# Optimization experiments

Hardware: AMD Instinct MI355X
Metric: run time of the kernel (lower is better)

The kernel has to match this reference:

```python
import jax, jax.numpy as jnp
import numpy as np

N = 100000   # nodes
E = 3200000  # edges (avg degree 32)
IN = 128     # in_channels
H = 128      # hidden_channels
G = 512      # graphs in batch


def setup_inputs() -> dict:
    key = jax.random.key(0)
    ks = jax.random.split(key, 8)
    x = jax.random.normal(ks[0], (N, IN), dtype=jnp.float32)
    edge_index = jax.random.randint(ks[1], (2, E), 0, N, dtype=jnp.int64)
    batch = jnp.sort(jax.random.randint(ks[2], (N,), 0, G, dtype=jnp.int64))
    s_in = 1.0 / np.sqrt(IN)
    s_h = 1.0 / np.sqrt(H)
    W1 = jax.random.normal(ks[3], (IN, H), dtype=jnp.float32) * s_in
    b1 = jnp.zeros((H,), dtype=jnp.float32)
    W2 = jax.random.normal(ks[4], (H, H), dtype=jnp.float32) * s_h
    b2 = jnp.zeros((H,), dtype=jnp.float32)
    Wc = jax.random.normal(ks[5], (H, 1), dtype=jnp.float32) * s_h
    bc = jnp.zeros((1,), dtype=jnp.float32)
    return {"x": x, "edge_index": edge_index, "batch": batch,
            "W1": W1, "b1": b1, "W2": W2, "b2": b2, "Wc": Wc, "bc": bc}


def _gcn_conv(x, W, b, src, dst, n):
    # PyG GCNConv: x' = D^{-1/2} (A+I) D^{-1/2} X W + b  (self-loops already in src/dst)
    h = x @ W                                      # [n, H] small GEMM
    ones = jnp.ones(src.shape[0], dtype=h.dtype)
    deg = jax.ops.segment_sum(ones, dst, num_segments=n)
    dinv = jnp.where(deg > 0, jax.lax.rsqrt(deg), 0.0)
    norm = dinv[src] * dinv[dst]                   # [E+n]
    msgs = h[src] * norm[:, None]                  # gather + scale (memory-bound)
    return jax.ops.segment_sum(msgs, dst, num_segments=n) + b


def reference(x, edge_index, batch, W1, b1, W2, b2, Wc, bc):
    n = x.shape[0]
    loop = jnp.arange(n, dtype=edge_index.dtype)
    src = jnp.concatenate([edge_index[0], loop])   # add self-loops
    dst = jnp.concatenate([edge_index[1], loop])
    h = jax.nn.relu(_gcn_conv(x, W1, b1, src, dst, n))
    h = jax.nn.relu(_gcn_conv(h, W2, b2, src, dst, n))
    # global_mean_pool: segment mean over graph ids
    counts = jax.ops.segment_sum(jnp.ones(n, dtype=h.dtype), batch, num_segments=G)
    sums = jax.ops.segment_sum(h, batch, num_segments=G)
    pooled = sums / jnp.maximum(counts, 1.0)[:, None]   # [G, H]
    return jax.nn.sigmoid(pooled @ Wc + bc)             # [G, 1]
```

## Files before the change

### kernel.cpp

```cpp
#include <hip/hip_runtime.h>

typedef unsigned short ushort_t;
typedef unsigned int uint_t;
typedef unsigned char u8_t;

typedef __bf16 bf16x8 __attribute__((ext_vector_type(8)));
typedef float f32x4 __attribute__((ext_vector_type(4)));
typedef uint_t uint32x4 __attribute__((ext_vector_type(4)));
typedef uint_t uint32x2 __attribute__((ext_vector_type(2)));
typedef _Float16 h2 __attribute__((ext_vector_type(2)));

#define EPB 5120
#define NSH 9
#define MSK 511
#define BPAD 4104

__device__ __forceinline__ float b2f(ushort_t u) {
    union { uint_t ui; float f; } c; c.ui = ((uint_t)u) << 16; return c.f;
}
__device__ __forceinline__ ushort_t f2b(float f) {
    union { float f; uint_t ui; } c; c.f = f;
    uint_t u = c.ui;
    uint_t r = (u + 0x7fffu + ((u >> 16) & 1u)) >> 16;
    return (ushort_t)r;
}
__device__ __forceinline__ u8_t f2e5(float x) {
    ushort_t h = __builtin_bit_cast(ushort_t, (_Float16)x);
    uint_t r = ((uint_t)h + 0x7Fu + ((h >> 8) & 1u)) >> 8;
    return (u8_t)r;
}
__device__ __forceinline__ void upk_add(uint_t d, h2* acc) {
    uint_t A = __builtin_amdgcn_perm(0u, d, 0x010C000Cu);
    uint_t B = __builtin_amdgcn_perm(0u, d, 0x030C020Cu);
    acc[0] += __builtin_bit_cast(h2, A);
    acc[1] += __builtin_bit_cast(h2, B);
}

__global__ __launch_bounds__(256) void p1_hist(const int* __restrict__ dst,
                                               int* __restrict__ H,
                                               const float* __restrict__ W1,
                                               const float* __restrict__ W2,
                                               ushort_t* __restrict__ W1t,
                                               ushort_t* __restrict__ W2t,
                                               u8_t* __restrict__ h8z,
                                               int E, int NBLK, int B, int N) {
    int t = threadIdx.x, c = blockIdx.x;
    if (c >= NBLK + 128) {
        if (t < 32) ((uint_t*)h8z)[(size_t)N * 32 + t] = 0u;
        return;
    }
    if (c >= NBLK) {
        int idx = (c - NBLK) * 256 + t;
        int sel = idx >> 14;
        int i = idx & 16383;
        int k = i >> 7, nn = i & 127;
        const float* S = sel ? W2 : W1;
        ushort_t* D = sel ? W2t : W1t;
        D[nn * 128 + k] = f2b(S[k * 128 + nn]);
        return;
    }
    __shared__ int hist[256];
    if (t < 256) hist[t] = 0;
    __syncthreads();
    int base = c * EPB;
    int lim = min(E - base, EPB);
    for (int i = t; i < lim; i += 256)
        atomicAdd(&hist[dst[base + i] >> NSH], 1);
    __syncthreads();
    if (t < B) H[t * NBLK + c] = hist[t];
}

__global__ __launch_bounds__(256) void reduce256(const int* __restrict__ in,
                                                 int* __restrict__ bsums, int n) {
    __shared__ int s[256];
    int t = threadIdx.x, g = blockIdx.x * 256 + t;
    s[t] = (g < n) ? in[g] : 0;
    __syncthreads();
    for (int o = 128; o > 0; o >>= 1) {
        if (t < o) s[t] += s[t + o];
        __syncthreads();
    }
    if (t == 0) bsums[blockIdx.x] = s[0];
}

__global__ __launch_bounds__(512) void scan_small(const int* __restrict__ in,
                                                  int* __restrict__ outEx, int n) {
    __shared__ int s[512];
    int t = threadIdx.x;
    int v = (t < n) ? in[t] : 0;
    s[t] = v;
    __syncthreads();
    for (int o = 1; o < 512; o <<= 1) {
        int x = 0;
        if (t >= o) x = s[t - o];
        __syncthreads();
        s[t] += x;
        __syncthreads();
    }
    if (t < n) outEx[t] = s[t] - v;
}

__global__ __launch_bounds__(256) void scan256ex(const int* __restrict__ in,
                                                 const int* __restrict__ boffs,
                                                 int* __restrict__ outEx, int n) {
    __shared__ int s[256];
    int t = threadIdx.x, g = blockIdx.x * 256 + t;
    int v = (g < n) ? in[g] : 0;
    s[t] = v;
    __syncthreads();
    for (int o = 1; o < 256; o <<= 1) {
        int x = 0;
        if (t >= o) x = s[t - o];
        __syncthreads();
        s[t] += x;
        __syncthreads();
    }
    if (g < n) outEx[g] = boffs[blockIdx.x] + s[t] - v;
}

__global__ __launch_bounds__(256) void p3_scatter(const int* __restrict__ src,
                                                  const int* __restrict__ dst,
                                                  const int* __restrict__ Hex,
                                                  uint_t* __restrict__ packed,
                                                  int E, int NBLK, int B) {
    __shared__ int offsL[256];
    __shared__ int cur[256];
    int t = threadIdx.x, c = blockIdx.x;
    if (t < B) {
        offsL[t] = Hex[t * NBLK + c];
        cur[t] = 0;
    }
    __syncthreads();
    int base = c * EPB;
    int lim = min(E - base, EPB);
    for (int i = t; i < lim; i += 256) {
        int d = dst[base + i];
        int s = src[base + i];
        int b = d >> NSH;
        int r = atomicAdd(&cur[b], 1);
        packed[offsL[b] + r] = ((uint_t)s << NSH) | (uint_t)(d & MSK);
    }
}

__global__ __launch_bounds__(512) void p4_build(const uint_t* __restrict__ packed,
                                                const int* __restrict__ Hex,
                                                int* __restrict__ adj,
                                                int* __restrict__ offs,
                                                int* __restrict__ dgr,
                                                float* __restrict__ dinv,
                                                int E, int N, int NBLK, int B) {
    __shared__ int dcnt[512], loc[512], cur[512], sps[512];
    int t = threadIdx.x, b = blockIdx.x;
    int bs = Hex[b * NBLK];
    int be = (b + 1 < B) ? Hex[(b + 1) * NBLK] : E;
    int m = be - bs;
    dcnt[t] = 0;
    __syncthreads();
    for (int i = t; i < m; i += 512)
        atomicAdd(&dcnt[packed[bs + i] & MSK], 1);
    __syncthreads();
    int d = dcnt[t];
    int pd = (d + 8) & ~7;
    sps[t] = pd;
    __syncthreads();
    for (int o = 1; o < 512; o <<= 1) {
        int x = 0;
        if (t >= o) x = sps[t - o];
        __syncthreads();
        sps[t] += x;
        __syncthreads();
    }
    int bsp = ((bs + 7) & ~7) + b * BPAD;
    int ex = sps[t] - pd;
    int node = b * 512 + t;
    if (node < N) {
        int nbase = bsp + ex;
        offs[node] = nbase;
        dgr[node]  = pd;
        dinv[node] = rsqrtf((float)(d + 1));
        adj[nbase] = node;
        for (int i = d + 1; i < pd; ++i)
            adj[nbase + i] = N;
    }
    loc[t] = ex + 1;
    cur[t] = 0;
    __syncthreads();
    for (int i = t; i < m; i += 512) {
        uint_t p = packed[bs + i];
        int l = p & MSK;
        int r = atomicAdd(&cur[l], 1);
        adj[bsp + loc[l] + r] = (int)(p >> NSH);
    }
}

__global__ __launch_bounds__(256, 4) void gemm_scale(const ushort_t* __restrict__ Xin,
                                                     const ushort_t* __restrict__ Wt,
                                                     const float* __restrict__ dinv,
                                                     u8_t* __restrict__ Hout8, int n) {
    __shared__ ushort_t lds[128 * 136];
    int tid = threadIdx.x;
    for (int i = tid; i < 128 * 16; i += 256) {
        int r = i >> 4, c8 = (i & 15) << 3;
        *(uint32x4*)(lds + r * 136 + c8) = *(const uint32x4*)(Wt + r * 128 + c8);
    }
    __syncthreads();
    int lane = tid & 63, wave = tid >> 6;
    int m = lane & 15, q = lane >> 4;
    int row0 = blockIdx.x * 64 + wave * 16;
    int ar = row0 + m;
    if (ar > n - 1) ar = n - 1;
    bf16x8 a[4];
#pragma unroll
    for (int ks = 0; ks < 4; ++ks)
        a[ks] = __builtin_bit_cast(bf16x8,
            *(const uint32x4*)(Xin + (size_t)ar * 128 + ks * 32 + q * 8));
    f32x4 acc[8];
    f32x4 zero = {0.f, 0.f, 0.f, 0.f};
#pragma unroll
    for (int nt = 0; nt < 8; ++nt) acc[nt] = zero;
#pragma unroll
    for (int nt = 0; nt < 8; ++nt) {
#pragma unroll
        for (int ks = 0; ks < 4; ++ks) {
            bf16x8 b = __builtin_bit_cast(bf16x8,
                *(const uint32x4*)(lds + (nt * 16 + m) * 136 + ks * 32 + q * 8));
            acc[nt] = __builtin_amdgcn_mfma_f32_16x16x32_bf16(a[ks], b, acc[nt], 0, 0, 0);
        }
    }
    float dv[4];
#pragma unroll
    for (int r = 0; r < 4; ++r) {
        int gr = row0 + q * 4 + r;
        dv[r] = (gr < n) ? dinv[gr] : 0.f;
    }
#pragma unroll
    for (int nt = 0; nt < 8; ++nt) {
#pragma unroll
        for (int r = 0; r < 4; ++r) {
            int gr = row0 + q * 4 + r;
            if (gr < n)
                Hout8[(size_t)gr * 128 + nt * 16 + m] = f2e5(acc[nt][r] * dv[r]);
        }
    }
}

__global__ __launch_bounds__(256, 4) void gemm_scale_f32(const float* __restrict__ Xf,
                                                         const ushort_t* __restrict__ Wt,
                                                         const float* __restrict__ dinv,
                                                         u8_t* __restrict__ Hout8, int n) {
    __shared__ ushort_t lds[128 * 136];
    int tid = threadIdx.x;
    for (int i = tid; i < 128 * 16; i += 256) {
        int r = i >> 4, c8 = (i & 15) << 3;
        *(uint32x4*)(lds + r * 136 + c8) = *(const uint32x4*)(Wt + r * 128 + c8);
    }
    __syncthreads();
    int lane = tid & 63, wave = tid >> 6;
    int m = lane & 15, q = lane >> 4;
    int row0 = blockIdx.x * 64 + wave * 16;
    int ar = row0 + m;
    if (ar > n - 1) ar = n - 1;
    bf16x8 a[4];
#pragma unroll
    for (int ks = 0; ks < 4; ++ks) {
        const float* p = Xf + (size_t)ar * 128 + ks * 32 + q * 8;
        f32x4 lo = *(const f32x4*)p;
        f32x4 hi = *(const f32x4*)(p + 4);
        ushort_t t[8];
        t[0] = f2b(lo[0]); t[1] = f2b(lo[1]); t[2] = f2b(lo[2]); t[3] = f2b(lo[3]);
        t[4] = f2b(hi[0]); t[5] = f2b(hi[1]); t[6] = f2b(hi[2]); t[7] = f2b(hi[3]);
        a[ks] = __builtin_bit_cast(bf16x8, *(uint32x4*)t);
    }
    f32x4 acc[8];
    f32x4 zero = {0.f, 0.f, 0.f, 0.f};
#pragma unroll
    for (int nt = 0; nt < 8; ++nt) acc[nt] = zero;
#pragma unroll
    for (int nt = 0; nt < 8; ++nt) {
#pragma unroll
        for (int ks = 0; ks < 4; ++ks) {
            bf16x8 b = __builtin_bit_cast(bf16x8,
                *(const uint32x4*)(lds + (nt * 16 + m) * 136 + ks * 32 + q * 8));
            acc[nt] = __builtin_amdgcn_mfma_f32_16x16x32_bf16(a[ks], b, acc[nt], 0, 0, 0);
        }
    }
    float dv[4];
#pragma unroll
    for (int r = 0; r < 4; ++r) {
        int gr = row0 + q * 4 + r;
        dv[r] = (gr < n) ? dinv[gr] : 0.f;
    }
#pragma unroll
    for (int nt = 0; nt < 8; ++nt) {
#pragma unroll
        for (int r = 0; r < 4; ++r) {
            int gr = row0 + q * 4 + r;
            if (gr < n)
                Hout8[(size_t)gr * 128 + nt * 16 + m] = f2e5(acc[nt][r] * dv[r]);
        }
    }
}

__device__ __forceinline__ void agg_core(const u8_t* __restrict__ Hs8,
                                         const int* __restrict__ adj,
                                         int beg, int pd, int g, uint_t colb,
                                         h2* acc) {
    int e = 0;
    for (; e + 16 <= pd; e += 16) {
        const int4 sv = *(const int4*)(adj + beg + e + g * 4);
        uint_t o0 = ((uint_t)sv.x << 7) | colb;
        uint_t o1 = ((uint_t)sv.y << 7) | colb;
        uint_t o2 = ((uint_t)sv.z << 7) | colb;
        uint_t o3 = ((uint_t)sv.w << 7) | colb;
        uint32x2 w0 = *(const uint32x2*)(Hs8 + o0);
        uint32x2 w1 = *(const uint32x2*)(Hs8 + o1);
        uint32x2 w2 = *(const uint32x2*)(Hs8 + o2);
        uint32x2 w3 = *(const uint32x2*)(Hs8 + o3);
        upk_add(w0[0], acc); upk_add(w0[1], acc + 2);
        upk_add(w1[0], acc); upk_add(w1[1], acc + 2);
        upk_add(w2[0], acc); upk_add(w2[1], acc + 2);
        upk_add(w3[0], acc); upk_add(w3[1], acc + 2);
    }
    if (e < pd) {
        const int2 sv = *(const int2*)(adj + beg + e + g * 2);
        uint_t o0 = ((uint_t)sv.x << 7) | colb;
        uint_t o1 = ((uint_t)sv.y << 7) | colb;
        uint32x2 w0 = *(const uint32x2*)(Hs8 + o0);
        uint32x2 w1 = *(const uint32x2*)(Hs8 + o1);
        upk_add(w0[0], acc); upk_add(w0[1], acc + 2);
        upk_add(w1[0], acc); upk_add(w1[1], acc + 2);
    }
}

__device__ __forceinline__ void slot_reduce(h2* acc) {
#pragma unroll
    for (int k = 0; k < 4; ++k) {
        uint_t v = __builtin_bit_cast(uint_t, acc[k]);
        acc[k] += __builtin_bit_cast(h2, (uint_t)__shfl_xor(v, 16, 64));
        v = __builtin_bit_cast(uint_t, acc[k]);
        acc[k] += __builtin_bit_cast(h2, (uint_t)__shfl_xor(v, 32, 64));
    }
}

__global__ __launch_bounds__(256, 4) void agg_kernel(const u8_t* __restrict__ Hs8,
                                                     const int* __restrict__ adj,
                                                     const int* __restrict__ offs,
                                                     const int* __restrict__ dgr,
                                                     const float* __restrict__ dinv,
                                                     const float* __restrict__ bias,
                                                     ushort_t* __restrict__ Out, int n) {
    int node = blockIdx.x * 4 + (threadIdx.x >> 6);
    if (node >= n) return;
    int lane = threadIdx.x & 63;
    int g = lane >> 4;
    int l16 = lane & 15;
    uint_t colb = (uint_t)l16 * 8;
    const int beg = offs[node];
    const int pd  = dgr[node];
    h2 acc[4];
    h2 hz = {(_Float16)0.f, (_Float16)0.f};
#pragma unroll
    for (int k = 0; k < 4; ++k) acc[k] = hz;
    agg_core(Hs8, adj, beg, pd, g, colb, acc);
    slot_reduce(acc);
    if (g == 0) {
        float di = dinv[node];
        ushort_t o[8];
#pragma unroll
        for (int k = 0; k < 4; ++k) {
            float f0 = (float)acc[k][0];
            float f1 = (float)acc[k][1];
            o[2 * k]     = f2b(fmaxf(di * f0 + bias[colb + 2 * k], 0.f));
            o[2 * k + 1] = f2b(fmaxf(di * f1 + bias[colb + 2 * k + 1], 0.f));
        }
        *(uint32x4*)(Out + (size_t)node * 128 + colb) = *(uint32x4*)o;
    }
}

__global__ __launch_bounds__(256, 4) void agg_pool_kernel(const u8_t* __restrict__ Hs8,
                                                          const int* __restrict__ adj,
                                                          const int* __restrict__ offs,
                                                          const int* __restrict__ dgr,
                                                          const float* __restrict__ dinv,
                                                          const float* __restrict__ bias,
                                                          const float* __restrict__ Wc,
                                                          float* __restrict__ Sout, int n) {
    int node = blockIdx.x * 4 + (threadIdx.x >> 6);
    if (node >= n) return;
    int lane = threadIdx.x & 63;
    int g = lane >> 4;
    int l16 = lane & 15;
    uint_t colb = (uint_t)l16 * 8;
    const int beg = offs[node];
    const int pd  = dgr[node];
    h2 acc[4];
    h2 hz = {(_Float16)0.f, (_Float16)0.f};
#pragma unroll
    for (int k = 0; k < 4; ++k) acc[k] = hz;
    agg_core(Hs8, adj, beg, pd, g, colb, acc);
    slot_reduce(acc);
    float local = 0.f;
    float di = dinv[node];
#pragma unroll
    for (int k = 0; k < 4; ++k) {
        float f0 = fmaxf(di * (float)acc[k][0] + bias[colb + 2 * k], 0.f);
        float f1 = fmaxf(di * (float)acc[k][1] + bias[colb + 2 * k + 1], 0.f);
        local += f0 * Wc[colb + 2 * k] + f1 * Wc[colb + 2 * k + 1];
    }
    local += __shfl_xor(local, 1, 64);
    local += __shfl_xor(local, 2, 64);
    local += __shfl_xor(local, 4, 64);
    local += __shfl_xor(local, 8, 64);
    if (lane == 0) Sout[node] = local;
}

__global__ __launch_bounds__(256) void pool2_kernel(const float* __restrict__ S,
                                                    const int* __restrict__ batch,
                                                    const float* __restrict__ bc,
                                                    float* __restrict__ out, int n) {
    int g = blockIdx.x;
    int t = threadIdx.x;
    int lo = 0, hi = n;
    while (lo < hi) { int mid = (lo + hi) >> 1; if (batch[mid] < g) lo = mid + 1; else hi = mid; }
    int start = lo;
    hi = n;
    while (lo < hi) { int mid = (lo + hi) >> 1; if (batch[mid] < g + 1) lo = mid + 1; else hi = mid; }
    int stop = lo;
    float s = 0.f;
    for (int i = start + t; i < stop; i += 256) s += S[i];
    __shared__ float red[256];
    red[t] = s;
    __syncthreads();
    for (int o = 128; o > 0; o >>= 1) {
        if (t < o) red[t] += red[t + o];
        __syncthreads();
    }
    if (t == 0) {
        int cg = stop - start;
        float z = red[0] / (float)(cg > 0 ? cg : 1) + bc[0];
        out[g] = 1.f / (1.f + expf(-z));
    }
}

extern "C" void kernel_launch(void* const* d_in, const int* in_sizes, int n_in,
                              void* d_out, int out_size, void* d_ws, size_t ws_size,
                              hipStream_t stream) {
    const float* X     = (const float*)d_in[0];
    const int* ei      = (const int*)d_in[1];
    const int* batch   = (const int*)d_in[2];
    const float* W1    = (const float*)d_in[3];
    const float* b1    = (const float*)d_in[4];
    const float* W2    = (const float*)d_in[5];
    const float* b2    = (const float*)d_in[6];
    const float* Wc    = (const float*)d_in[7];
    const float* bc    = (const float*)d_in[8];

    const int N = in_sizes[2];
    const int E = in_sizes[1] / 2;
    const int G = out_size;
    const int* srcv = ei;
    const int* dstv = ei + E;

    const int NBLK = (E + EPB - 1) / EPB;
    const int B    = (N + MSK) >> NSH;
    const int n0   = B * NBLK;
    const int g1   = (n0 + 255) / 256;

    char* p = (char*)d_ws;
    auto alloc = [&](size_t bytes) -> void* {
        void* r = (void*)p;
        p += (bytes + 255) & ~(size_t)255;
        return r;
    };
    int* H         = (int*)alloc((size_t)n0 * 4);
    int* Hex       = (int*)alloc((size_t)n0 * 4);
    int* S1        = (int*)alloc((size_t)g1 * 4);
    int* S1ex      = (int*)alloc((size_t)g1 * 4);
    uint_t* packed = (uint_t*)alloc((size_t)E * 4);
    int* adj       = (int*)alloc(((size_t)E + (size_t)B * BPAD + 4224) * 4);
    int* offs      = (int*)alloc(((size_t)N + 1) * 4);
    int* dgr       = (int*)alloc((size_t)N * 4);
    float* dinv    = (float*)alloc((size_t)N * 4);
    ushort_t* W1t  = (ushort_t*)alloc(16384 * 2);
    ushort_t* W2t  = (ushort_t*)alloc(16384 * 2);
    u8_t* h8       = (u8_t*)alloc(((size_t)N + 1) * 128);
    ushort_t* bufA = (ushort_t*)alloc((size_t)N * 128 * 2);
    float* Snode   = (float*)alloc((size_t)N * 4);

    p1_hist<<<NBLK + 129, 256, 0, stream>>>(dstv, H, W1, W2, W1t, W2t, h8, E, NBLK, B, N);
    reduce256<<<g1, 256, 0, stream>>>(H, S1, n0);
    scan_small<<<1, 512, 0, stream>>>(S1, S1ex, g1);
    scan256ex<<<g1, 256, 0, stream>>>(H, S1ex, Hex, n0);
    p3_scatter<<<NBLK, 256, 0, stream>>>(srcv, dstv, Hex, packed, E, NBLK, B);
    p4_build<<<B, 512, 0, stream>>>(packed, Hex, adj, offs, dgr, dinv, E, N, NBLK, B);

    const int GB = (N + 63) / 64;
    const int AB = (N + 3) / 4;
    gemm_scale_f32<<<GB, 256, 0, stream>>>(X, W1t, dinv, h8, N);
    agg_kernel<<<AB, 256, 0, stream>>>(h8, adj, offs, dgr, dinv, b1, bufA, N);
    gemm_scale<<<GB, 256, 0, stream>>>(bufA, W2t, dinv, h8, N);
    agg_pool_kernel<<<AB, 256, 0, stream>>>(h8, adj, offs, dgr, dinv, b2, Wc, Snode, N);
    pool2_kernel<<<G, 256, 0, stream>>>(Snode, batch, bc, (float*)d_out, N);
}
```

Before: 339.6 us.

## Store layer-1 output as fp8 e5m2, use f16 MFMA, fuse pooling via atomics

The first aggregation now writes its ReLU output as 8-bit e5m2 instead of bf16. The second GEMM unpacks those bytes into f16 and runs f16 MFMA against an f16-converted W2, which halves the intermediate activation traffic. The per-node pooled scalars are accumulated directly into per-graph sums with atomics, so the Snode buffer and the block reduction in the final kernel go away. The cost is lower precision in the hidden activations and atomic contention on 512 graph sums.

```diff
diff --git a/kernel.cpp b/kernel.cpp
--- a/kernel.cpp
+++ b/kernel.cpp
@@ -5,6 +5,7 @@
 typedef unsigned char u8_t;
 
 typedef __bf16 bf16x8 __attribute__((ext_vector_type(8)));
+typedef _Float16 f16x8 __attribute__((ext_vector_type(8)));
 typedef float f32x4 __attribute__((ext_vector_type(4)));
 typedef uint_t uint32x4 __attribute__((ext_vector_type(4)));
 typedef uint_t uint32x2 __attribute__((ext_vector_type(2)));
@@ -43,10 +44,12 @@
                                                ushort_t* __restrict__ W1t,
                                                ushort_t* __restrict__ W2t,
                                                u8_t* __restrict__ h8z,
-                                               int E, int NBLK, int B, int N) {
+                                               float* __restrict__ gsum,
+                                               int E, int NBLK, int B, int N, int G) {
     int t = threadIdx.x, c = blockIdx.x;
     if (c >= NBLK + 128) {
         if (t < 32) ((uint_t*)h8z)[(size_t)N * 32 + t] = 0u;
+        for (int i = t; i < G; i += 256) gsum[i] = 0.f;
         return;
     }
     if (c >= NBLK) {
@@ -54,9 +57,11 @@
         int sel = idx >> 14;
         int i = idx & 16383;
         int k = i >> 7, nn = i & 127;
-        const float* S = sel ? W2 : W1;
-        ushort_t* D = sel ? W2t : W1t;
-        D[nn * 128 + k] = f2b(S[k * 128 + nn]);
+        if (sel) {
+            W2t[nn * 128 + k] = __builtin_bit_cast(ushort_t, (_Float16)W2[k * 128 + nn]);
+        } else {
+            W1t[nn * 128 + k] = f2b(W1[k * 128 + nn]);
+        }
         return;
     }
     __shared__ int hist[256];
@@ -193,7 +198,7 @@
     }
 }
 
-__global__ __launch_bounds__(256, 4) void gemm_scale(const ushort_t* __restrict__ Xin,
+__global__ __launch_bounds__(256, 4) void gemm_scale(const u8_t* __restrict__ Xin8,
                                                      const ushort_t* __restrict__ Wt,
                                                      const float* __restrict__ dinv,
                                                      u8_t* __restrict__ Hout8, int n) {
@@ -209,11 +214,17 @@
     int row0 = blockIdx.x * 64 + wave * 16;
     int ar = row0 + m;
     if (ar > n - 1) ar = n - 1;
-    bf16x8 a[4];
-#pragma unroll
-    for (int ks = 0; ks < 4; ++ks)
-        a[ks] = __builtin_bit_cast(bf16x8,
-            *(const uint32x4*)(Xin + (size_t)ar * 128 + ks * 32 + q * 8));
+    f16x8 a[4];
+#pragma unroll
+    for (int ks = 0; ks < 4; ++ks) {
+        uint32x2 dv8 = *(const uint32x2*)(Xin8 + (size_t)ar * 128 + ks * 32 + q * 8);
+        uint_t tw[4];
+        tw[0] = __builtin_amdgcn_perm(0u, dv8[0], 0x010C000Cu);
+        tw[1] = __builtin_amdgcn_perm(0u, dv8[0], 0x030C020Cu);
+        tw[2] = __builtin_amdgcn_perm(0u, dv8[1], 0x010C000Cu);
+        tw[3] = __builtin_amdgcn_perm(0u, dv8[1], 0x030C020Cu);
+        a[ks] = __builtin_bit_cast(f16x8, *(uint32x4*)tw);
+    }
     f32x4 acc[8];
     f32x4 zero = {0.f, 0.f, 0.f, 0.f};
 #pragma unroll
@@ -222,9 +233,9 @@
     for (int nt = 0; nt < 8; ++nt) {
 #pragma unroll
         for (int ks = 0; ks < 4; ++ks) {
-            bf16x8 b = __builtin_bit_cast(bf16x8,
+            f16x8 b = __builtin_bit_cast(f16x8,
                 *(const uint32x4*)(lds + (nt * 16 + m) * 136 + ks * 32 + q * 8));
-            acc[nt] = __builtin_amdgcn_mfma_f32_16x16x32_bf16(a[ks], b, acc[nt], 0, 0, 0);
+            acc[nt] = __builtin_amdgcn_mfma_f32_16x16x32_f16(a[ks], b, acc[nt], 0, 0, 0);
         }
     }
     float dv[4];
@@ -348,7 +359,7 @@
                                                      const int* __restrict__ dgr,
                                                      const float* __restrict__ dinv,
                                                      const float* __restrict__ bias,
-                                                     ushort_t* __restrict__ Out, int n) {
+                                                     u8_t* __restrict__ Out8, int n) {
     int node = blockIdx.x * 4 + (threadIdx.x >> 6);
     if (node >= n) return;
     int lane = threadIdx.x & 63;
@@ -365,15 +376,15 @@
     slot_reduce(acc);
     if (g == 0) {
         float di = dinv[node];
-        ushort_t o[8];
+        u8_t o[8];
 #pragma unroll
         for (int k = 0; k < 4; ++k) {
             float f0 = (float)acc[k][0];
             float f1 = (float)acc[k][1];
-            o[2 * k]     = f2b(fmaxf(di * f0 + bias[colb + 2 * k], 0.f));
-            o[2 * k + 1] = f2b(fmaxf(di * f1 + bias[colb + 2 * k + 1], 0.f));
+            o[2 * k]     = f2e5(fmaxf(di * f0 + bias[colb + 2 * k], 0.f));
+            o[2 * k + 1] = f2e5(fmaxf(di * f1 + bias[colb + 2 * k + 1], 0.f));
         }
-        *(uint32x4*)(Out + (size_t)node * 128 + colb) = *(uint32x4*)o;
+        *(uint32x2*)(Out8 + (size_t)node * 128 + colb) = *(uint32x2*)o;
     }
 }
 
@@ -384,7 +395,8 @@
                                                           const float* __restrict__ dinv,
                                                           const float* __restrict__ bias,
                                                           const float* __restrict__ Wc,
-                                                          float* __restrict__ Sout, int n) {
+                                                          const int* __restrict__ batch,
+                                                          float* __restrict__ gsum, int n) {
     int node = blockIdx.x * 4 + (threadIdx.x >> 6);
     if (node >= n) return;
     int lane = threadIdx.x & 63;
@@ -411,35 +423,23 @@
     local += __shfl_xor(local, 2, 64);
     local += __shfl_xor(local, 4, 64);
     local += __shfl_xor(local, 8, 64);
-    if (lane == 0) Sout[node] = local;
-}
-
-__global__ __launch_bounds__(256) void pool2_kernel(const float* __restrict__ S,
-                                                    const int* __restrict__ batch,
-                                                    const float* __restrict__ bc,
-                                                    float* __restrict__ out, int n) {
-    int g = blockIdx.x;
-    int t = threadIdx.x;
+    if (lane == 0) atomicAdd(&gsum[batch[node]], local);
+}
+
+__global__ __launch_bounds__(512) void pool_fin(const float* __restrict__ gsum,
+                                                const int* __restrict__ batch,
+                                                const float* __restrict__ bc,
+                                                float* __restrict__ out, int n, int G) {
+    int g = blockIdx.x * 512 + threadIdx.x;
+    if (g >= G) return;
     int lo = 0, hi = n;
     while (lo < hi) { int mid = (lo + hi) >> 1; if (batch[mid] < g) lo = mid + 1; else hi = mid; }
     int start = lo;
     hi = n;
     while (lo < hi) { int mid = (lo + hi) >> 1; if (batch[mid] < g + 1) lo = mid + 1; else hi = mid; }
-    int stop = lo;
-    float s = 0.f;
-    for (int i = start + t; i < stop; i += 256) s += S[i];
-    __shared__ float red[256];
-    red[t] = s;
-    __syncthreads();
-    for (int o = 128; o > 0; o >>= 1) {
-        if (t < o) red[t] += red[t + o];
-        __syncthreads();
-    }
-    if (t == 0) {
-        int cg = stop - start;
-        float z = red[0] / (float)(cg > 0 ? cg : 1) + bc[0];
-        out[g] = 1.f / (1.f + expf(-z));
-    }
+    int cnt = lo - start;
+    float z = gsum[g] / (float)(cnt > 0 ? cnt : 1) + bc[0];
+    out[g] = 1.f / (1.f + expf(-z));
 }
 
 extern "C" void kernel_launch(void* const* d_in, const int* in_sizes, int n_in,
@@ -484,10 +484,11 @@
     ushort_t* W1t  = (ushort_t*)alloc(16384 * 2);
     ushort_t* W2t  = (ushort_t*)alloc(16384 * 2);
     u8_t* h8       = (u8_t*)alloc(((size_t)N + 1) * 128);
-    ushort_t* bufA = (ushort_t*)alloc((size_t)N * 128 * 2);
-    float* Snode   = (float*)alloc((size_t)N * 4);
-
-    p1_hist<<<NBLK + 129, 256, 0, stream>>>(dstv, H, W1, W2, W1t, W2t, h8, E, NBLK, B, N);
+    u8_t* h8b      = (u8_t*)alloc((size_t)N * 128);
+    float* gsum    = (float*)alloc((size_t)(G > 512 ? G : 512) * 4);
+
+    p1_hist<<<NBLK + 129, 256, 0, stream>>>(dstv, H, W1, W2, W1t, W2t, h8, gsum,
+                                            E, NBLK, B, N, G);
     reduce256<<<g1, 256, 0, stream>>>(H, S1, n0);
     scan_small<<<1, 512, 0, stream>>>(S1, S1ex, g1);
     scan256ex<<<g1, 256, 0, stream>>>(H, S1ex, Hex, n0);
@@ -497,8 +498,9 @@
     const int GB = (N + 63) / 64;
     const int AB = (N + 3) / 4;
     gemm_scale_f32<<<GB, 256, 0, stream>>>(X, W1t, dinv, h8, N);
-    agg_kernel<<<AB, 256, 0, stream>>>(h8, adj, offs, dgr, dinv, b1, bufA, N);
-    gemm_scale<<<GB, 256, 0, stream>>>(bufA, W2t, dinv, h8, N);
-    agg_pool_kernel<<<AB, 256, 0, stream>>>(h8, adj, offs, dgr, dinv, b2, Wc, Snode, N);
-    pool2_kernel<<<G, 256, 0, stream>>>(Snode, batch, bc, (float*)d_out, N);
-}
+    agg_kernel<<<AB, 256, 0, stream>>>(h8, adj, offs, dgr, dinv, b1, h8b, N);
+    gemm_scale<<<GB, 256, 0, stream>>>(h8b, W2t, dinv, h8, N);
+    agg_pool_kernel<<<AB, 256, 0, stream>>>(h8, adj, offs, dgr, dinv, b2, Wc,
+                                            batch, gsum, N);
+    pool_fin<<<(G + 511) / 512, 512, 0, stream>>>(gsum, batch, bc, (float*)d_out, N, G);
+}
```

Measured after the change: 573.1 us. +68.8%, slower.
